# Kernel optimization log

Hardware: AMD Instinct MI355X
Metric: run time of the kernel (lower is better)

The kernel has to match this reference:

```python
import jax, jax.numpy as jnp
import numpy as np

B, T, D, H = 128, 100, 4096, 256


def setup_inputs() -> dict:
    key = jax.random.key(0)
    ks = jax.random.split(key, 8)
    def xavier(k, shape):
        fan_in, fan_out = shape
        limit = float(np.sqrt(6.0 / (fan_in + fan_out)))
        return jax.random.uniform(k, shape, jnp.float32, -limit, limit)
    x = (jax.random.uniform(ks[0], (B, T, D), jnp.float32) < 0.1).astype(jnp.float32)  # sparse baskets
    return {
        "x": x,
        "W_fx": xavier(ks[1], (D, H)),
        "W_fh": xavier(ks[2], (H, H)),
        "b_f": jnp.zeros((H,), jnp.float32),
        "W_mx": xavier(ks[3], (D, H)),
        "W_mh": xavier(ks[4], (H, H)),
        "b_m": jnp.zeros((H,), jnp.float32),
        "W_cx": xavier(ks[5], (D, H)),
        "W_ch": xavier(ks[6], (H, H)),
        "b_c": jnp.zeros((H,), jnp.float32),
        "W_ph": xavier(ks[7], (H, D)),
        "b_p": jnp.zeros((D,), jnp.float32),
    }


def reference(x, W_fx, W_fh, b_f, W_mx, W_mh, b_m, W_cx, W_ch, b_c, W_ph, b_p):
    # Precompute all input projections in one big GEMM per gate: [B,T,H]
    xf = jnp.einsum("btd,dh->bth", x, W_fx) + b_f
    xm = jnp.einsum("btd,dh->bth", x, W_mx) + b_m
    xc = jnp.einsum("btd,dh->bth", x, W_cx) + b_c

    def step(hidden, inp):
        xf_t, xm_t, xc_t = inp  # each [B, H]
        forget = jax.nn.sigmoid(xf_t + hidden @ W_fh)
        modul = jax.nn.sigmoid(xm_t + hidden @ W_mh)
        cand = jnp.tanh(xc_t + (hidden * modul) @ W_ch)
        hidden = hidden * (1.0 - forget) + forget * cand
        return hidden, hidden

    h0 = jnp.zeros((B, H), x.dtype)
    # scan over time: inputs shaped [T, B, H]
    xs = (xf.transpose(1, 0, 2), xm.transpose(1, 0, 2), xc.transpose(1, 0, 2))
    _, hiddens = jax.lax.scan(step, h0, xs)  # [T, B, H]
    hiddens = hiddens.transpose(1, 0, 2)  # [B, T, H]
    pred_sequence = jax.nn.sigmoid(jnp.einsum("bth,hd->btd", hiddens, W_ph) + b_p)
    return pred_sequence
```

## Files before the change

### kernel.cpp

```cpp
#include <hip/hip_runtime.h>
#include <hip/hip_bf16.h>

#define B_  128
#define T_  100
#define D_  4096
#define H_  256
#define NF  768

typedef __attribute__((ext_vector_type(4))) float f32x4;
typedef __attribute__((ext_vector_type(8))) short s16x8;
typedef __attribute__((ext_vector_type(8))) _Float16 f16x8;
typedef __attribute__((ext_vector_type(4))) int v4i;

#define WLIM 0.10825317547305482
#define QW   ((float)(32512.0 / WLIM))
#define QH2F 32512.0f
#define MAGICF 12615808.0f
#define SS2  (WLIM / (32512.0 * 32512.0))
#define C16F ((float)(SS2 * 65536.0))
#define C8F  ((float)(SS2 * 256.0))

#define HSTR 272
#define FSTR 260
#define XPST 772

static __device__ __forceinline__ unsigned short f2bf(float f) {
  unsigned u = __builtin_bit_cast(unsigned, f);
  unsigned r = (u + 0x7fffu + ((u >> 16) & 1u)) >> 16;
  return (unsigned short)r;
}
static __device__ __forceinline__ float bf2f(unsigned short u) {
  unsigned v = ((unsigned)u) << 16;
  return __builtin_bit_cast(float, v);
}
static __device__ __forceinline__ unsigned short f2h(float f) {
  _Float16 h = (_Float16)f;
  return __builtin_bit_cast(unsigned short, h);
}
static __device__ __forceinline__ float sigmoidf_(float x) {
  return 1.0f / (1.0f + __expf(-x));
}
static __device__ __forceinline__ float tanhf_(float x) {
  return 2.0f / (1.0f + __expf(-2.0f * x)) - 1.0f;
}
static __device__ __forceinline__ void async16(const void* g, void* l) {
  __builtin_amdgcn_global_load_lds(
      (const __attribute__((address_space(1))) unsigned*)g,
      (__attribute__((address_space(3))) unsigned*)l, 16, 0, 0);
}
static __device__ __forceinline__ f32x4 mfma_bf(s16x8 a, s16x8 b, f32x4 c) {
  return __builtin_amdgcn_mfma_f32_16x16x32_bf16(a, b, c, 0, 0, 0);
}
static __device__ __forceinline__ f32x4 mfma_f16(f16x8 a, f16x8 b, f32x4 c) {
  return __builtin_amdgcn_mfma_f32_16x16x32_f16(a, b, c, 0, 0, 0);
}
static __device__ __forceinline__ v4i mfma_i8x64(v4i a, v4i b, v4i c) {
  return __builtin_amdgcn_mfma_i32_16x16x64_i8(a, b, c, 0, 0, 0);
}
static __device__ __forceinline__ void pack2planes(const float* v, unsigned& phi,
                                                   unsigned& plo) {
  unsigned u0 = __builtin_bit_cast(unsigned, fmaf(v[0], QH2F, MAGICF));
  unsigned u1 = __builtin_bit_cast(unsigned, fmaf(v[1], QH2F, MAGICF));
  unsigned u2 = __builtin_bit_cast(unsigned, fmaf(v[2], QH2F, MAGICF));
  unsigned u3 = __builtin_bit_cast(unsigned, fmaf(v[3], QH2F, MAGICF));
  unsigned t01h = __builtin_amdgcn_perm(u1, u0, 0x00000501u);
  unsigned t23h = __builtin_amdgcn_perm(u3, u2, 0x05010000u);
  unsigned t01l = __builtin_amdgcn_perm(u1, u0, 0x00000400u);
  unsigned t23l = __builtin_amdgcn_perm(u3, u2, 0x04000000u);
  phi = __builtin_amdgcn_perm(t23h, t01h, 0x07060100u) ^ 0x80808080u;
  plo = __builtin_amdgcn_perm(t23l, t01l, 0x07060100u) ^ 0x80808080u;
}

__global__ void pack_bias(const float* __restrict__ bf, const float* __restrict__ bm,
                          const float* __restrict__ bc, float* __restrict__ out) {
  int i = threadIdx.x;
  out[i] = (i < 256) ? bf[i] : (i < 512 ? bm[i - 256] : bc[i - 512]);
}

__global__ void transpose_cvt_f16(const float* __restrict__ src,
                                  unsigned short* __restrict__ dst, int R, int C) {
  __shared__ float tile[32][33];
  int tx = threadIdx.x, ty = threadIdx.y;
  int rb = blockIdx.y * 32, cb = blockIdx.x * 32;
#pragma unroll
  for (int i = 0; i < 4; ++i)
    tile[ty + 8 * i][tx] = src[(size_t)(rb + ty + 8 * i) * C + cb + tx];
  __syncthreads();
#pragma unroll
  for (int i = 0; i < 4; ++i)
    dst[(size_t)(cb + ty + 8 * i) * R + rb + tx] = f2h(tile[tx][ty + 8 * i]);
}

__global__ void transpose_cvt_hilo(const float* __restrict__ s0, const float* __restrict__ s1,
                                   const float* __restrict__ s2,
                                   unsigned short* __restrict__ dhi,
                                   unsigned short* __restrict__ dlo, int R, int C) {
  __shared__ float tile[32][33];
  const float* src = (blockIdx.z == 0) ? s0 : (blockIdx.z == 1 ? s1 : s2);
  size_t goff = (size_t)blockIdx.z * (size_t)R * (size_t)C;
  int tx = threadIdx.x, ty = threadIdx.y;
  int rb = blockIdx.y * 32, cb = blockIdx.x * 32;
#pragma unroll
  for (int i = 0; i < 4; ++i)
    tile[ty + 8 * i][tx] = src[(size_t)(rb + ty + 8 * i) * C + cb + tx];
  __syncthreads();
#pragma unroll
  for (int i = 0; i < 4; ++i) {
    float w = tile[tx][ty + 8 * i];
    unsigned short hi = f2bf(w);
    float lo = w - bf2f(hi);
    size_t idx = goff + (size_t)(cb + ty + 8 * i) * R + rb + tx;
    dhi[idx] = hi;
    dlo[idx] = f2bf(lo);
  }
}

__global__ void wh_prep(const float* __restrict__ s0, const float* __restrict__ s1,
                        const float* __restrict__ s2, signed char* __restrict__ ph,
                        signed char* __restrict__ pl) {
  int g = blockIdx.x, tx = threadIdx.x;
  const float* src = (g == 0) ? s0 : (g == 1 ? s1 : s2);
  int col = g * 256 + tx;
  for (int k = 0; k < 256; ++k) {
    float w = src[k * 256 + tx];
    int wq = (int)rintf(w * QW);
    int wh = (wq + 128) >> 8;
    int wl = wq - (wh << 8);
    ph[col * 256 + k] = (signed char)wh;
    pl[col * 256 + k] = (signed char)wl;
  }
}

__global__ __launch_bounds__(256) void gemm_xproj(
    const float* __restrict__ X, const unsigned short* __restrict__ Wh,
    const unsigned short* __restrict__ Wl, const float* __restrict__ bias,
    float* __restrict__ out) {
  __shared__ unsigned short As[128 * 32];
  __shared__ unsigned short Bh[128 * 32];
  __shared__ unsigned short Bl[128 * 32];
  const int tid = threadIdx.x;
  const int mbase = blockIdx.y * 128, nbase = blockIdx.x * 128;
  const int lane = tid & 63, wv = tid >> 6;
  const int q = lane >> 4, l16 = lane & 15;
  const int mh = (wv >> 1) * 64, nh = (wv & 1) * 64;
  const int srow = tid >> 2, scol = (tid & 3) * 8;

  f32x4 acc[4][4];
#pragma unroll
  for (int a = 0; a < 4; ++a)
#pragma unroll
    for (int b = 0; b < 4; ++b) acc[a][b] = (f32x4)0.0f;

  for (int kt = 0; kt < D_ / 32; ++kt) {
    const int k0 = kt * 32;
#pragma unroll
    for (int p = 0; p < 2; ++p) {
      const float* ag = X + (size_t)(mbase + srow + p * 64) * D_ + k0 + scol;
      float4 f0 = *(const float4*)ag;
      float4 f1 = *(const float4*)(ag + 4);
      uint4 pk;
      pk.x = f2bf(f0.x) | ((unsigned)f2bf(f0.y) << 16);
      pk.y = f2bf(f0.z) | ((unsigned)f2bf(f0.w) << 16);
      pk.z = f2bf(f1.x) | ((unsigned)f2bf(f1.y) << 16);
      pk.w = f2bf(f1.z) | ((unsigned)f2bf(f1.w) << 16);
      *(uint4*)((char*)As + tid * 16 + p * 4096) = pk;
    }
#pragma unroll
    for (int p = 0; p < 2; ++p) {
      size_t boff = (size_t)(nbase + srow + p * 64) * D_ + k0 + scol;
      async16(Wh + boff, (char*)Bh + tid * 16 + p * 4096);
      async16(Wl + boff, (char*)Bl + tid * 16 + p * 4096);
    }
    __syncthreads();
    s16x8 af[4], bh[4], bl[4];
#pragma unroll
    for (int mt = 0; mt < 4; ++mt)
      af[mt] = *(const s16x8*)((char*)As + (mh + mt * 16 + l16) * 64 + q * 16);
#pragma unroll
    for (int nt = 0; nt < 4; ++nt) {
      bh[nt] = *(const s16x8*)((char*)Bh + (nh + nt * 16 + l16) * 64 + q * 16);
      bl[nt] = *(const s16x8*)((char*)Bl + (nh + nt * 16 + l16) * 64 + q * 16);
    }
#pragma unroll
    for (int mt = 0; mt < 4; ++mt)
#pragma unroll
      for (int nt = 0; nt < 4; ++nt) {
        acc[mt][nt] = mfma_bf(af[mt], bh[nt], acc[mt][nt]);
        acc[mt][nt] = mfma_bf(af[mt], bl[nt], acc[mt][nt]);
      }
    __syncthreads();
  }
#pragma unroll
  for (int mt = 0; mt < 4; ++mt)
#pragma unroll
    for (int nt = 0; nt < 4; ++nt) {
      int gc = nbase + nh + nt * 16 + l16;
      float bv = bias[gc];
#pragma unroll
      for (int i = 0; i < 4; ++i) {
        int gr = mbase + mh + mt * 16 + q * 4 + i;
        out[(size_t)gr * NF + gc] = acc[mt][nt][i] + bv;
      }
    }
}

__global__ __launch_bounds__(256) void gemm_out(
    const unsigned short* __restrict__ Hm, const unsigned short* __restrict__ Wt,
    const float* __restrict__ bias, float* __restrict__ out) {
  __shared__ unsigned short As[128 * 32];
  __shared__ unsigned short Bs[128 * 32];
  const int tid = threadIdx.x;
  const int mbase = blockIdx.y * 128, nbase = blockIdx.x * 128;
  const int lane = tid & 63, wv = tid >> 6;
  const int q = lane >> 4, l16 = lane & 15;
  const int mh = (wv >> 1) * 64, nh = (wv & 1) * 64;
  const int srow = tid >> 2, scol = (tid & 3) * 8;

  f32x4 acc[4][4];
#pragma unroll
  for (int a = 0; a < 4; ++a)
#pragma unroll
    for (int b = 0; b < 4; ++b) acc[a][b] = (f32x4)0.0f;

  for (int kt = 0; kt < H_ / 32; ++kt) {
    const int k0 = kt * 32;
#pragma unroll
    for (int p = 0; p < 2; ++p) {
      async16(Hm + (size_t)(mbase + srow + p * 64) * H_ + k0 + scol,
              (char*)As + tid * 16 + p * 4096);
      async16(Wt + (size_t)(nbase + srow + p * 64) * H_ + k0 + scol,
              (char*)Bs + tid * 16 + p * 4096);
    }
    __syncthreads();
    f16x8 af[4], bf[4];
#pragma unroll
    for (int mt = 0; mt < 4; ++mt)
      af[mt] = *(const f16x8*)((char*)As + (mh + mt * 16 + l16) * 64 + q * 16);
#pragma unroll
    for (int nt = 0; nt < 4; ++nt)
      bf[nt] = *(const f16x8*)((char*)Bs + (nh + nt * 16 + l16) * 64 + q * 16);
#pragma unroll
    for (int mt = 0; mt < 4; ++mt)
#pragma unroll
      for (int nt = 0; nt < 4; ++nt)
        acc[mt][nt] = mfma_f16(af[mt], bf[nt], acc[mt][nt]);
    __syncthreads();
  }
#pragma unroll
  for (int mt = 0; mt < 4; ++mt)
#pragma unroll
    for (int nt = 0; nt < 4; ++nt) {
      int gc = nbase + nh + nt * 16 + l16;
      float bv = bias[gc];
#pragma unroll
      for (int i = 0; i < 4; ++i) {
        int gr = mbase + mh + mt * 16 + q * 4 + i;
        float v = acc[mt][nt][i] + bv;
        out[(size_t)gr * D_ + gc] = 1.0f / (1.0f + __expf(-v));
      }
    }
}

__global__ __launch_bounds__(512, 2) void scan_kernel(
    const float* __restrict__ xproj,
    const signed char* __restrict__ wph,
    const signed char* __restrict__ wpl,
    unsigned short* __restrict__ hid) {
  __shared__ __align__(16) signed char hA[2][16 * HSTR];
  __shared__ __align__(16) signed char gA[2][16 * HSTR];
  __shared__ __align__(16) float hbuf[16 * FSTR];
  __shared__ __align__(16) float fbuf[16 * FSTR];
  __shared__ __align__(16) float xp[2][16 * XPST];

  const int tid = threadIdx.x;
  const int wv = tid >> 6, lane = tid & 63;
  const int q = lane >> 4, l16 = lane & 15;
  const int rb = blockIdx.x * 16;

  int tb[6];
  tb[0] = (2 * wv) * 16;
  tb[1] = tb[0] + 16;
  tb[2] = 256 + tb[0];
  tb[3] = 256 + tb[1];
  tb[4] = 512 + tb[0];
  tb[5] = 512 + tb[1];

  v4i wrh[6][4], wrl[6][4];
#pragma unroll
  for (int s = 0; s < 6; ++s)
#pragma unroll
    for (int ch = 0; ch < 4; ++ch) {
      size_t o = (size_t)(tb[s] + l16) * 256 + ch * 64 + q * 16;
      wrh[s][ch] = *(const v4i*)(wph + o);
      wrl[s][ch] = *(const v4i*)(wpl + o);
    }

  float hr[8];
#pragma unroll
  for (int j = 0; j < 8; ++j) hr[j] = 0.0f;

  for (int i = tid; i < 16 * FSTR; i += 512) hbuf[i] = 0.0f;
  for (int i = tid; i < 2 * 16 * HSTR; i += 512) ((signed char*)hA)[i] = 0;
#pragma unroll
  for (int p = 0; p < 6; ++p) {
    int s = wv * 6 + p;
    int row = s / 3, part = s - row * 3;
    async16(xproj + (size_t)(rb + row) * T_ * NF + part * 256 + lane * 4,
            (char*)&xp[0][0] + row * (XPST * 4) + part * 1024 + lane * 16);
  }
  __syncthreads();

  for (int t = 0; t < T_; ++t) {
    const float* xcur = &xp[t & 1][0];
#pragma unroll
    for (int half = 0; half < 2; ++half) {
      v4i a[2][2];
#pragma unroll
      for (int s2 = 0; s2 < 2; ++s2) {
        a[s2][0] = (v4i){0, 0, 0, 0};
        a[s2][1] = (v4i){0, 0, 0, 0};
      }
      __builtin_amdgcn_s_setprio(1);
#pragma unroll
      for (int ch = 0; ch < 4; ++ch) {
        int ao = l16 * HSTR + ch * 64 + q * 16;
        v4i bh = *(const v4i*)&hA[0][ao];
        v4i bl = *(const v4i*)&hA[1][ao];
#pragma unroll
        for (int s2 = 0; s2 < 2; ++s2) {
          int s = half * 2 + s2;
          a[s2][0] = mfma_i8x64(wrh[s][ch], bh, a[s2][0]);
          a[s2][1] = mfma_i8x64(wrl[s][ch], bh, a[s2][1]);
          a[s2][1] = mfma_i8x64(wrh[s][ch], bl, a[s2][1]);
        }
      }
      __builtin_amdgcn_s_setprio(0);
#pragma unroll
      for (int s2 = 0; s2 < 2; ++s2) {
        int s = half * 2 + s2;
        int cb = tb[s] + q * 4;
        float4 xv = *(const float4*)&xcur[l16 * XPST + cb];
        float xx4[4] = {xv.x, xv.y, xv.z, xv.w};
        float pre[4];
#pragma unroll
        for (int i = 0; i < 4; ++i)
          pre[i] = xx4[i] + (float)a[s2][0][i] * C16F + (float)a[s2][1][i] * C8F;
        if (half == 0) {
          float4 fv = make_float4(sigmoidf_(pre[0]), sigmoidf_(pre[1]),
                                  sigmoidf_(pre[2]), sigmoidf_(pre[3]));
          *(float4*)&fbuf[l16 * FSTR + cb] = fv;
        } else {
          int cm = cb - 256;
          float4 hv = *(const float4*)&hbuf[l16 * FSTR + cm];
          float gg[4] = {hv.x * sigmoidf_(pre[0]), hv.y * sigmoidf_(pre[1]),
                         hv.z * sigmoidf_(pre[2]), hv.w * sigmoidf_(pre[3])};
          unsigned phi, plo;
          pack2planes(gg, phi, plo);
          *(unsigned*)&gA[0][l16 * HSTR + cm] = phi;
          *(unsigned*)&gA[1][l16 * HSTR + cm] = plo;
        }
      }
    }
    __syncthreads();

    {
      int tt = (t + 1 < T_) ? (t + 1) : (T_ - 1);
      char* dst = (char*)&xp[(t + 1) & 1][0];
#pragma unroll
      for (int p = 0; p < 6; ++p) {
        int s = wv * 6 + p;
        int row = s / 3, part = s - row * 3;
        async16(xproj + ((size_t)(rb + row) * T_ + tt) * NF + part * 256 + lane * 4,
                dst + row * (XPST * 4) + part * 1024 + lane * 16);
      }
    }

    {
      v4i b[2][2];
#pragma unroll
      for (int s2 = 0; s2 < 2; ++s2) {
        b[s2][0] = (v4i){0, 0, 0, 0};
        b[s2][1] = (v4i){0, 0, 0, 0};
      }
      __builtin_amdgcn_s_setprio(1);
#pragma unroll
      for (int ch = 0; ch < 4; ++ch) {
        int ao = l16 * HSTR + ch * 64 + q * 16;
        v4i gh_ = *(const v4i*)&gA[0][ao];
        v4i gl_ = *(const v4i*)&gA[1][ao];
#pragma unroll
        for (int s2 = 0; s2 < 2; ++s2) {
          int s = 4 + s2;
          b[s2][0] = mfma_i8x64(wrh[s][ch], gh_, b[s2][0]);
          b[s2][1] = mfma_i8x64(wrl[s][ch], gh_, b[s2][1]);
          b[s2][1] = mfma_i8x64(wrh[s][ch], gl_, b[s2][1]);
        }
      }
      __builtin_amdgcn_s_setprio(0);
#pragma unroll
      for (int s2 = 0; s2 < 2; ++s2) {
        int cc = tb[4 + s2] - 512 + q * 4;
        float4 xv = *(const float4*)&xcur[l16 * XPST + 512 + cc];
        float4 fv = *(const float4*)&fbuf[l16 * FSTR + cc];
        float xx4[4] = {xv.x, xv.y, xv.z, xv.w};
        float ff4[4] = {fv.x, fv.y, fv.z, fv.w};
        float hn[4];
#pragma unroll
        for (int i = 0; i < 4; ++i) {
          float pre = xx4[i] + (float)b[s2][0][i] * C16F + (float)b[s2][1][i] * C8F;
          float c = tanhf_(pre);
          float h = hr[s2 * 4 + i];
          h += ff4[i] * (c - h);
          hr[s2 * 4 + i] = h;
          hn[i] = h;
        }
        unsigned phi, plo;
        pack2planes(hn, phi, plo);
        *(unsigned*)&hA[0][l16 * HSTR + cc] = phi;
        *(unsigned*)&hA[1][l16 * HSTR + cc] = plo;
        *(float4*)&hbuf[l16 * FSTR + cc] = make_float4(hn[0], hn[1], hn[2], hn[3]);
        unsigned u0 = f2h(hn[0]) | ((unsigned)f2h(hn[1]) << 16);
        unsigned u1 = f2h(hn[2]) | ((unsigned)f2h(hn[3]) << 16);
        *(uint2*)&hid[((size_t)(rb + l16) * T_ + t) * H_ + cc] = make_uint2(u0, u1);
      }
    }
    __syncthreads();
  }
}

extern "C" void kernel_launch(void* const* d_in, const int* in_sizes, int n_in,
                              void* d_out, int out_size, void* d_ws, size_t ws_size,
                              hipStream_t stream) {
  const float* x   = (const float*)d_in[0];
  const float* Wfx = (const float*)d_in[1];
  const float* Wfh = (const float*)d_in[2];
  const float* bf  = (const float*)d_in[3];
  const float* Wmx = (const float*)d_in[4];
  const float* Wmh = (const float*)d_in[5];
  const float* bm  = (const float*)d_in[6];
  const float* Wcx = (const float*)d_in[7];
  const float* Wch = (const float*)d_in[8];
  const float* bc  = (const float*)d_in[9];
  const float* Wph = (const float*)d_in[10];
  const float* bp  = (const float*)d_in[11];
  float* out = (float*)d_out;

  char* ws = (char*)d_ws;
  unsigned short* WxHi = (unsigned short*)ws;
  unsigned short* WxLo = (unsigned short*)(ws + 6291456);
  unsigned short* WphT = (unsigned short*)(ws + 12582912);
  signed char* WhP     = (signed char*)(ws + 14680064);
  signed char* WlP     = (signed char*)(ws + 14876672);
  float* bfused        = (float*)(ws + 15076352);
  float* xproj         = (float*)(ws + 15079424);
  unsigned short* hid  = (unsigned short*)(ws + 54401024);

  transpose_cvt_hilo<<<dim3(8, 128, 3), dim3(32, 8), 0, stream>>>(
      Wfx, Wmx, Wcx, WxHi, WxLo, 4096, 256);
  transpose_cvt_f16<<<dim3(128, 8), dim3(32, 8), 0, stream>>>(Wph, WphT, 256, 4096);
  wh_prep<<<3, 256, 0, stream>>>(Wfh, Wmh, Wch, WhP, WlP);
  pack_bias<<<1, 768, 0, stream>>>(bf, bm, bc, bfused);
  gemm_xproj<<<dim3(6, 100), 256, 0, stream>>>(x, WxHi, WxLo, bfused, xproj);
  scan_kernel<<<8, 512, 0, stream>>>(xproj, WhP, WlP, hid);
  gemm_out<<<dim3(32, 100), 256, 0, stream>>>(hid, WphT, bp, out);
}
```

Baseline: 1.258 ms.

## Restructure scan kernel to 16 waves with fused gate math and pre-negated projections

The recurrent scan kernel moves from 8 to 16 waves per block. Each wave now owns one 16-column slice of every gate, so the forget and modulation MFMAs share B-operand loads, and the forget gate stays in registers instead of going through an LDS buffer. The input-projection GEMM pre-scales its outputs by -1 or -2 so the sigmoid/tanh can be computed with a single fma, exp and rcp, and the two int8 accumulator planes are combined in integer arithmetic. The wh_prep weight-quantization kernel is split across more blocks. The goal is shorter per-step latency on the serial scan, at the cost of more register pressure per wave and a dependence on the pre-negated xproj layout.

```diff
diff --git a/kernel.cpp b/kernel.cpp
--- a/kernel.cpp
+++ b/kernel.cpp
@@ -17,12 +17,14 @@
 #define QH2F 32512.0f
 #define MAGICF 12615808.0f
 #define SS2  (WLIM / (32512.0 * 32512.0))
-#define C16F ((float)(SS2 * 65536.0))
-#define C8F  ((float)(SS2 * 256.0))
+#define C8D  (SS2 * 256.0)
 
 #define HSTR 272
-#define FSTR 260
+#define PLSTR (16 * HSTR)
+#define SLOT  (2 * PLSTR)
+#define GAOFF (2 * SLOT)
 #define XPST 772
+#define XPBYTES (16 * XPST * 4)
 
 static __device__ __forceinline__ unsigned short f2bf(float f) {
   unsigned u = __builtin_bit_cast(unsigned, f);
@@ -36,12 +38,6 @@
 static __device__ __forceinline__ unsigned short f2h(float f) {
   _Float16 h = (_Float16)f;
   return __builtin_bit_cast(unsigned short, h);
-}
-static __device__ __forceinline__ float sigmoidf_(float x) {
-  return 1.0f / (1.0f + __expf(-x));
-}
-static __device__ __forceinline__ float tanhf_(float x) {
-  return 2.0f / (1.0f + __expf(-2.0f * x)) - 1.0f;
 }
 static __device__ __forceinline__ void async16(const void* g, void* l) {
   __builtin_amdgcn_global_load_lds(
@@ -118,10 +114,10 @@
 __global__ void wh_prep(const float* __restrict__ s0, const float* __restrict__ s1,
                         const float* __restrict__ s2, signed char* __restrict__ ph,
                         signed char* __restrict__ pl) {
-  int g = blockIdx.x, tx = threadIdx.x;
+  int g = blockIdx.x, kb = blockIdx.y * 32, tx = threadIdx.x;
   const float* src = (g == 0) ? s0 : (g == 1 ? s1 : s2);
   int col = g * 256 + tx;
-  for (int k = 0; k < 256; ++k) {
+  for (int k = kb; k < kb + 32; ++k) {
     float w = src[k * 256 + tx];
     int wq = (int)rintf(w * QW);
     int wh = (wq + 128) >> 8;
@@ -196,10 +192,11 @@
     for (int nt = 0; nt < 4; ++nt) {
       int gc = nbase + nh + nt * 16 + l16;
       float bv = bias[gc];
+      float s = (gc < 512) ? -1.0f : -2.0f;
 #pragma unroll
       for (int i = 0; i < 4; ++i) {
         int gr = mbase + mh + mt * 16 + q * 4 + i;
-        out[(size_t)gr * NF + gc] = acc[mt][nt][i] + bv;
+        out[(size_t)gr * NF + gc] = (acc[mt][nt][i] + bv) * s;
       }
     }
 }
@@ -261,15 +258,12 @@
     }
 }
 
-__global__ __launch_bounds__(512, 2) void scan_kernel(
+__global__ __launch_bounds__(1024, 4) void scan_kernel(
     const float* __restrict__ xproj,
     const signed char* __restrict__ wph,
     const signed char* __restrict__ wpl,
     unsigned short* __restrict__ hid) {
-  __shared__ __align__(16) signed char hA[2][16 * HSTR];
-  __shared__ __align__(16) signed char gA[2][16 * HSTR];
-  __shared__ __align__(16) float hbuf[16 * FSTR];
-  __shared__ __align__(16) float fbuf[16 * FSTR];
+  __shared__ __align__(16) signed char enc[3 * SLOT];
   __shared__ __align__(16) float xp[2][16 * XPST];
 
   const int tid = threadIdx.x;
@@ -277,152 +271,119 @@
   const int q = lane >> 4, l16 = lane & 15;
   const int rb = blockIdx.x * 16;
 
-  int tb[6];
-  tb[0] = (2 * wv) * 16;
-  tb[1] = tb[0] + 16;
-  tb[2] = 256 + tb[0];
-  tb[3] = 256 + tb[1];
-  tb[4] = 512 + tb[0];
-  tb[5] = 512 + tb[1];
-
-  v4i wrh[6][4], wrl[6][4];
-#pragma unroll
-  for (int s = 0; s < 6; ++s)
+  const float C8FM = -(float)C8D;
+  const float C8C = -(float)(2.0 * C8D);
+
+  v4i wfh[4], wfl[4], wmh[4], wml[4], wch[4], wcl[4];
+#pragma unroll
+  for (int ch = 0; ch < 4; ++ch) {
+    size_t of = (size_t)(wv * 16 + l16) * 256 + ch * 64 + q * 16;
+    wfh[ch] = *(const v4i*)(wph + of);
+    wfl[ch] = *(const v4i*)(wpl + of);
+    wmh[ch] = *(const v4i*)(wph + of + 256 * 256);
+    wml[ch] = *(const v4i*)(wpl + of + 256 * 256);
+    wch[ch] = *(const v4i*)(wph + of + 512 * 256);
+    wcl[ch] = *(const v4i*)(wpl + of + 512 * 256);
+  }
+
+  float hr[4] = {0.0f, 0.0f, 0.0f, 0.0f};
+
+  for (int i = tid; i < SLOT; i += 1024) enc[i] = 0;
+
+  const int rdb = l16 * HSTR + q * 16;
+  const int wrb = l16 * HSTR + wv * 16 + q * 4;
+  const int xrb = l16 * (XPST * 4) + wv * 64 + q * 16;
+
+#pragma unroll
+  for (int p = 0; p < 3; ++p)
+    async16(xproj + (size_t)(rb + wv) * T_ * NF + p * 256 + lane * 4,
+            (char*)&xp[0][0] + wv * (XPST * 4) + p * 1024 + lane * 16);
+  __syncthreads();
+
+  for (int t = 0; t < T_; ++t) {
+    const int par = t & 1;
+    const int curS = par * SLOT, nxtS = SLOT - curS;
+    const int curX = par * XPBYTES, nxtX = XPBYTES - curX;
+    const char* xb = (const char*)&xp[0][0];
+
+    v4i m0 = (v4i){0, 0, 0, 0}, m1 = (v4i){0, 0, 0, 0};
+    v4i f0 = (v4i){0, 0, 0, 0}, f1 = (v4i){0, 0, 0, 0};
+    __builtin_amdgcn_s_setprio(1);
 #pragma unroll
     for (int ch = 0; ch < 4; ++ch) {
-      size_t o = (size_t)(tb[s] + l16) * 256 + ch * 64 + q * 16;
-      wrh[s][ch] = *(const v4i*)(wph + o);
-      wrl[s][ch] = *(const v4i*)(wpl + o);
-    }
-
-  float hr[8];
-#pragma unroll
-  for (int j = 0; j < 8; ++j) hr[j] = 0.0f;
-
-  for (int i = tid; i < 16 * FSTR; i += 512) hbuf[i] = 0.0f;
-  for (int i = tid; i < 2 * 16 * HSTR; i += 512) ((signed char*)hA)[i] = 0;
-#pragma unroll
-  for (int p = 0; p < 6; ++p) {
-    int s = wv * 6 + p;
-    int row = s / 3, part = s - row * 3;
-    async16(xproj + (size_t)(rb + row) * T_ * NF + part * 256 + lane * 4,
-            (char*)&xp[0][0] + row * (XPST * 4) + part * 1024 + lane * 16);
-  }
-  __syncthreads();
-
-  for (int t = 0; t < T_; ++t) {
-    const float* xcur = &xp[t & 1][0];
-#pragma unroll
-    for (int half = 0; half < 2; ++half) {
-      v4i a[2][2];
-#pragma unroll
-      for (int s2 = 0; s2 < 2; ++s2) {
-        a[s2][0] = (v4i){0, 0, 0, 0};
-        a[s2][1] = (v4i){0, 0, 0, 0};
+      v4i bh = *(const v4i*)&enc[curS + rdb + ch * 64];
+      v4i bl = *(const v4i*)&enc[curS + PLSTR + rdb + ch * 64];
+      m0 = mfma_i8x64(wmh[ch], bh, m0);
+      m1 = mfma_i8x64(wml[ch], bh, m1);
+      m1 = mfma_i8x64(wmh[ch], bl, m1);
+      f0 = mfma_i8x64(wfh[ch], bh, f0);
+      f1 = mfma_i8x64(wfl[ch], bh, f1);
+      f1 = mfma_i8x64(wfh[ch], bl, f1);
+    }
+    __builtin_amdgcn_s_setprio(0);
+    {
+      float4 zm = *(const float4*)(xb + curX + xrb + 1024);
+      float zz[4] = {zm.x, zm.y, zm.z, zm.w};
+      float g4[4];
+#pragma unroll
+      for (int i = 0; i < 4; ++i) {
+        int ti = (m0[i] << 8) + m1[i];
+        float w = fmaf((float)ti, C8FM, zz[i]);
+        float mg = __builtin_amdgcn_rcpf(1.0f + __expf(w));
+        g4[i] = hr[i] * mg;
       }
-      __builtin_amdgcn_s_setprio(1);
-#pragma unroll
-      for (int ch = 0; ch < 4; ++ch) {
-        int ao = l16 * HSTR + ch * 64 + q * 16;
-        v4i bh = *(const v4i*)&hA[0][ao];
-        v4i bl = *(const v4i*)&hA[1][ao];
-#pragma unroll
-        for (int s2 = 0; s2 < 2; ++s2) {
-          int s = half * 2 + s2;
-          a[s2][0] = mfma_i8x64(wrh[s][ch], bh, a[s2][0]);
-          a[s2][1] = mfma_i8x64(wrl[s][ch], bh, a[s2][1]);
-          a[s2][1] = mfma_i8x64(wrh[s][ch], bl, a[s2][1]);
-        }
-      }
-      __builtin_amdgcn_s_setprio(0);
-#pragma unroll
-      for (int s2 = 0; s2 < 2; ++s2) {
-        int s = half * 2 + s2;
-        int cb = tb[s] + q * 4;
-        float4 xv = *(const float4*)&xcur[l16 * XPST + cb];
-        float xx4[4] = {xv.x, xv.y, xv.z, xv.w};
-        float pre[4];
-#pragma unroll
-        for (int i = 0; i < 4; ++i)
-          pre[i] = xx4[i] + (float)a[s2][0][i] * C16F + (float)a[s2][1][i] * C8F;
-        if (half == 0) {
-          float4 fv = make_float4(sigmoidf_(pre[0]), sigmoidf_(pre[1]),
-                                  sigmoidf_(pre[2]), sigmoidf_(pre[3]));
-          *(float4*)&fbuf[l16 * FSTR + cb] = fv;
-        } else {
-          int cm = cb - 256;
-          float4 hv = *(const float4*)&hbuf[l16 * FSTR + cm];
-          float gg[4] = {hv.x * sigmoidf_(pre[0]), hv.y * sigmoidf_(pre[1]),
-                         hv.z * sigmoidf_(pre[2]), hv.w * sigmoidf_(pre[3])};
-          unsigned phi, plo;
-          pack2planes(gg, phi, plo);
-          *(unsigned*)&gA[0][l16 * HSTR + cm] = phi;
-          *(unsigned*)&gA[1][l16 * HSTR + cm] = plo;
-        }
-      }
+      unsigned phi, plo;
+      pack2planes(g4, phi, plo);
+      *(unsigned*)&enc[GAOFF + wrb] = phi;
+      *(unsigned*)&enc[GAOFF + PLSTR + wrb] = plo;
     }
     __syncthreads();
 
     {
       int tt = (t + 1 < T_) ? (t + 1) : (T_ - 1);
-      char* dst = (char*)&xp[(t + 1) & 1][0];
-#pragma unroll
-      for (int p = 0; p < 6; ++p) {
-        int s = wv * 6 + p;
-        int row = s / 3, part = s - row * 3;
-        async16(xproj + ((size_t)(rb + row) * T_ + tt) * NF + part * 256 + lane * 4,
-                dst + row * (XPST * 4) + part * 1024 + lane * 16);
+      const float* gsrc = xproj + ((size_t)(rb + wv) * T_ + tt) * NF + lane * 4;
+      char* dst = (char*)&xp[0][0] + nxtX + wv * (XPST * 4) + lane * 16;
+#pragma unroll
+      for (int p = 0; p < 3; ++p) async16(gsrc + p * 256, dst + p * 1024);
+    }
+
+    v4i c0 = (v4i){0, 0, 0, 0}, c1 = (v4i){0, 0, 0, 0};
+    __builtin_amdgcn_s_setprio(1);
+#pragma unroll
+    for (int ch = 0; ch < 4; ++ch) {
+      v4i gh = *(const v4i*)&enc[GAOFF + rdb + ch * 64];
+      v4i gl = *(const v4i*)&enc[GAOFF + PLSTR + rdb + ch * 64];
+      c0 = mfma_i8x64(wch[ch], gh, c0);
+      c1 = mfma_i8x64(wcl[ch], gh, c1);
+      c1 = mfma_i8x64(wch[ch], gl, c1);
+    }
+    __builtin_amdgcn_s_setprio(0);
+    {
+      float4 zc = *(const float4*)(xb + curX + xrb + 2048);
+      float4 zf = *(const float4*)(xb + curX + xrb);
+      float zc4[4] = {zc.x, zc.y, zc.z, zc.w};
+      float zf4[4] = {zf.x, zf.y, zf.z, zf.w};
+      float hn[4];
+#pragma unroll
+      for (int i = 0; i < 4; ++i) {
+        int tic = (c0[i] << 8) + c1[i];
+        float wc = fmaf((float)tic, C8C, zc4[i]);
+        float cv = fmaf(2.0f, __builtin_amdgcn_rcpf(1.0f + __expf(wc)), -1.0f);
+        int tif = (f0[i] << 8) + f1[i];
+        float wf = fmaf((float)tif, C8FM, zf4[i]);
+        float fv = __builtin_amdgcn_rcpf(1.0f + __expf(wf));
+        float h = fmaf(fv, cv - hr[i], hr[i]);
+        hr[i] = h;
+        hn[i] = h;
       }
-    }
-
-    {
-      v4i b[2][2];
-#pragma unroll
-      for (int s2 = 0; s2 < 2; ++s2) {
-        b[s2][0] = (v4i){0, 0, 0, 0};
-        b[s2][1] = (v4i){0, 0, 0, 0};
-      }
-      __builtin_amdgcn_s_setprio(1);
-#pragma unroll
-      for (int ch = 0; ch < 4; ++ch) {
-        int ao = l16 * HSTR + ch * 64 + q * 16;
-        v4i gh_ = *(const v4i*)&gA[0][ao];
-        v4i gl_ = *(const v4i*)&gA[1][ao];
-#pragma unroll
-        for (int s2 = 0; s2 < 2; ++s2) {
-          int s = 4 + s2;
-          b[s2][0] = mfma_i8x64(wrh[s][ch], gh_, b[s2][0]);
-          b[s2][1] = mfma_i8x64(wrl[s][ch], gh_, b[s2][1]);
-          b[s2][1] = mfma_i8x64(wrh[s][ch], gl_, b[s2][1]);
-        }
-      }
-      __builtin_amdgcn_s_setprio(0);
-#pragma unroll
-      for (int s2 = 0; s2 < 2; ++s2) {
-        int cc = tb[4 + s2] - 512 + q * 4;
-        float4 xv = *(const float4*)&xcur[l16 * XPST + 512 + cc];
-        float4 fv = *(const float4*)&fbuf[l16 * FSTR + cc];
-        float xx4[4] = {xv.x, xv.y, xv.z, xv.w};
-        float ff4[4] = {fv.x, fv.y, fv.z, fv.w};
-        float hn[4];
-#pragma unroll
-        for (int i = 0; i < 4; ++i) {
-          float pre = xx4[i] + (float)b[s2][0][i] * C16F + (float)b[s2][1][i] * C8F;
-          float c = tanhf_(pre);
-          float h = hr[s2 * 4 + i];
-          h += ff4[i] * (c - h);
-          hr[s2 * 4 + i] = h;
-          hn[i] = h;
-        }
-        unsigned phi, plo;
-        pack2planes(hn, phi, plo);
-        *(unsigned*)&hA[0][l16 * HSTR + cc] = phi;
-        *(unsigned*)&hA[1][l16 * HSTR + cc] = plo;
-        *(float4*)&hbuf[l16 * FSTR + cc] = make_float4(hn[0], hn[1], hn[2], hn[3]);
-        unsigned u0 = f2h(hn[0]) | ((unsigned)f2h(hn[1]) << 16);
-        unsigned u1 = f2h(hn[2]) | ((unsigned)f2h(hn[3]) << 16);
-        *(uint2*)&hid[((size_t)(rb + l16) * T_ + t) * H_ + cc] = make_uint2(u0, u1);
-      }
+      unsigned phi, plo;
+      pack2planes(hn, phi, plo);
+      *(unsigned*)&enc[nxtS + wrb] = phi;
+      *(unsigned*)&enc[nxtS + PLSTR + wrb] = plo;
+      unsigned u0 = __builtin_bit_cast(unsigned, __builtin_amdgcn_cvt_pkrtz(hn[0], hn[1]));
+      unsigned u1 = __builtin_bit_cast(unsigned, __builtin_amdgcn_cvt_pkrtz(hn[2], hn[3]));
+      *(uint2*)&hid[((size_t)(rb + l16) * T_ + t) * H_ + wv * 16 + q * 4] =
+          make_uint2(u0, u1);
     }
     __syncthreads();
   }
@@ -458,9 +419,9 @@
   transpose_cvt_hilo<<<dim3(8, 128, 3), dim3(32, 8), 0, stream>>>(
       Wfx, Wmx, Wcx, WxHi, WxLo, 4096, 256);
   transpose_cvt_f16<<<dim3(128, 8), dim3(32, 8), 0, stream>>>(Wph, WphT, 256, 4096);
-  wh_prep<<<3, 256, 0, stream>>>(Wfh, Wmh, Wch, WhP, WlP);
+  wh_prep<<<dim3(3, 8), 256, 0, stream>>>(Wfh, Wmh, Wch, WhP, WlP);
   pack_bias<<<1, 768, 0, stream>>>(bf, bm, bc, bfused);
   gemm_xproj<<<dim3(6, 100), 256, 0, stream>>>(x, WxHi, WxLo, bfused, xproj);
-  scan_kernel<<<8, 512, 0, stream>>>(xproj, WhP, WlP, hid);
+  scan_kernel<<<8, 1024, 0, stream>>>(xproj, WhP, WlP, hid);
   gemm_out<<<dim3(32, 100), 256, 0, stream>>>(hid, WphT, bp, out);
 }
```

Result: faster. 1.007 ms (-20.0%).
